# Kernel optimization log

Measured on AMD Instinct MI355X. Metric: run time of the kernel, lower is better.

Reference implementation:

```python
import jax, jax.numpy as jnp
import numpy as np

H = 32        # num query heads
KVH = 8       # num kv heads
D = 128       # head_dim
ROPE_BASE = 10000.0
NEG_INF = jnp.finfo(jnp.float32).min


def rope_interleaved(x):
    """Interleaved (GPT-NeoX-style pairs (x0,x1),(x2,x3),...) RoPE. x: [b,s,h,d]."""
    d = x.shape[-1]
    inv_freq = 1.0 / (ROPE_BASE ** (jnp.arange(0, d, 2, dtype=jnp.float32) / d))  # [d/2]
    pos = jnp.arange(x.shape[1], dtype=jnp.float32)
    ang = pos[:, None] * inv_freq[None, :]                    # [s, d/2]
    cos = jnp.cos(ang)[None, :, None, :]
    sin = jnp.sin(ang)[None, :, None, :]
    xp = x.reshape(*x.shape[:-1], d // 2, 2)
    x1, x2 = xp[..., 0], xp[..., 1]
    r1 = x1 * cos - x2 * sin
    r2 = x1 * sin + x2 * cos
    return jnp.stack([r1, r2], axis=-1).reshape(x.shape)


def setup_inputs() -> dict:
    key = jax.random.key(0)
    k1, k2, k3 = jax.random.split(key, 3)
    B, S, E = 2, 2048, 4096
    x = jax.random.normal(k1, (B, S, E), dtype=jnp.float32)
    wqkv = jax.random.normal(k2, (E + 2 * KVH * D, E), dtype=jnp.float32) * 0.02
    wo = jax.random.normal(k3, (E, E), dtype=jnp.float32) * 0.02
    return {"x": x, "wqkv": wqkv, "wo": wo}


def reference(x, wqkv, wo):
    b, s, e = x.shape
    q_per_kv = H // KVH
    # fused QKV projection (torch Linear layout: y = x @ W.T)
    qkv = jnp.einsum('bse,fe->bsf', x, wqkv)
    # rearrange 'b s (h gs d) -> b s h gs d', gs = q_per_kv + 2
    qkv = qkv.reshape(b, s, KVH, q_per_kv + 2, D)
    q = qkv[..., :q_per_kv, :].reshape(b, s, H, D)   # (h gs) -> H query heads
    k = qkv[..., -2, :]                              # [b,s,KVH,D]
    v = qkv[..., -1, :]
    # RoPE (rotary_emb_dim == head_dim, interleaved)
    q = rope_interleaved(q)
    k = rope_interleaved(k)
    # GQA: expand kv heads to match query heads
    k = jnp.repeat(k, q_per_kv, axis=2)              # [b,s,H,D]
    v = jnp.repeat(v, q_per_kv, axis=2)
    scale = D ** -0.5
    scores = jnp.einsum('bqhd,bkhd->bhqk', q, k) * scale
    causal = jnp.tril(jnp.ones((s, s), dtype=bool))
    scores = jnp.where(causal[None, None], scores, NEG_INF)
    attn = jax.nn.softmax(scores, axis=-1)
    ctx = jnp.einsum('bhqk,bkhd->bqhd', attn, v).reshape(b, s, H * D)
    return jnp.einsum('bsf,ef->bse', ctx, wo)
```

## Files before the change

kernel.cpp:

```cpp
#include <hip/hip_runtime.h>
#include <cstdint>

typedef __bf16 bf16;
typedef __bf16 bf16x8 __attribute__((ext_vector_type(8)));
typedef float  f32x4  __attribute__((ext_vector_type(4)));

#define AS1(p) ((__attribute__((address_space(1))) void*)(p))
#define AS3(p) ((__attribute__((address_space(3))) void*)(p))

__device__ __forceinline__ void gload16(const void* g, void* l) {
  __builtin_amdgcn_global_load_lds(AS1(g), AS3(l), 16, 0, 0);
}

constexpr int B_ = 2, S_ = 2048, E_ = 4096, H_ = 32, KVH_ = 8, D_ = 128;
constexpr int QPK_ = H_ / KVH_;
constexpr int F_ = E_ + 2 * KVH_ * D_;
constexpr int M_ = B_ * S_;

__global__ void f2bf_k(const float* __restrict__ in, bf16* __restrict__ out, int n8) {
  int i = blockIdx.x * 256 + threadIdx.x;
  if (i >= n8) return;
  const float4* p = (const float4*)(in + (size_t)i * 8);
  float4 a = p[0], b = p[1];
  bf16x8 o;
  o[0] = (bf16)a.x; o[1] = (bf16)a.y; o[2] = (bf16)a.z; o[3] = (bf16)a.w;
  o[4] = (bf16)b.x; o[5] = (bf16)b.y; o[6] = (bf16)b.z; o[7] = (bf16)b.w;
  *(bf16x8*)(out + (size_t)i * 8) = o;
}

__global__ void rope_table_k(float2* __restrict__ tab) {
  int i = blockIdx.x * 256 + threadIdx.x;
  int s = i >> 6, f = i & 63;
  float inv = powf(10000.0f, -2.0f * (float)f / 128.0f);
  float ang = (float)s * inv;
  tab[i] = make_float2(cosf(ang), sinf(ang));
}

template <typename OutT>
__global__ __launch_bounds__(512, 2)
void gemm128(const bf16* __restrict__ A, const bf16* __restrict__ B,
             OutT* __restrict__ C, int M, int N, int K) {
  __shared__ bf16 As[3][128 * 64];
  __shared__ bf16 Bs[3][256 * 64];
  const int tid = threadIdx.x;
  const int wid = tid >> 6, lane = tid & 63;
  const int l15 = lane & 15, g = lane >> 4;
  const int wr = wid >> 2, wc = wid & 3;
  const int bm = blockIdx.x, bn = blockIdx.y;
  const bf16* Ab = A + (size_t)bm * 128 * K;
  const bf16* Bb = B + (size_t)bn * 256 * K;
  const int nT = K >> 6;
  const int swzr = (l15 & 7) << 4;

  f32x4 acc[4][4];
#pragma unroll
  for (int m = 0; m < 4; ++m)
#pragma unroll
    for (int n = 0; n < 4; ++n) acc[m][n] = (f32x4){0.f, 0.f, 0.f, 0.f};

  auto stgA = [&](int t) {
    bf16* dst = &As[t % 3][0];
#pragma unroll
    for (int i = 0; i < 2; ++i) {
      int lb = i * 8192 + tid * 16;
      int row = lb >> 7;
      int colb = (lb & 127) ^ ((row & 7) << 4);
      gload16(Ab + (size_t)row * K + t * 64 + (colb >> 1),
              dst + ((i * 8192 + wid * 1024) >> 1));
    }
  };
  auto stgB = [&](int t) {
    bf16* dst = &Bs[t % 3][0];
#pragma unroll
    for (int i = 0; i < 4; ++i) {
      int lb = i * 8192 + tid * 16;
      int row = lb >> 7;
      int colb = (lb & 127) ^ ((row & 7) << 4);
      gload16(Bb + (size_t)row * K + t * 64 + (colb >> 1),
              dst + ((i * 8192 + wid * 1024) >> 1));
    }
  };

  stgA(0); stgB(0);
  if (nT > 1) { stgA(1); stgB(1); asm volatile("s_waitcnt vmcnt(6)"); }
  else        { asm volatile("s_waitcnt vmcnt(0)"); }
  __builtin_amdgcn_sched_barrier(0);
  __builtin_amdgcn_s_barrier();

  bf16x8 af[4][2], blo[2][2], bhi[2][2];
  for (int t = 0; t < nT; ++t) {
    const int cur = t % 3;
#pragma unroll
    for (int m = 0; m < 4; ++m) {
      int arow = wr * 64 + m * 16 + l15;
#pragma unroll
      for (int ks = 0; ks < 2; ++ks)
        af[m][ks] = *(const bf16x8*)&As[cur][(arow << 6) + (((ks * 64 + g * 16) ^ swzr) >> 1)];
    }
#pragma unroll
    for (int n = 0; n < 2; ++n) {
      int brow = wc * 64 + n * 16 + l15;
#pragma unroll
      for (int ks = 0; ks < 2; ++ks)
        blo[n][ks] = *(const bf16x8*)&Bs[cur][(brow << 6) + (((ks * 64 + g * 16) ^ swzr) >> 1)];
    }
    if (t + 2 < nT) stgA(t + 2);
    __builtin_amdgcn_s_barrier();
    asm volatile("s_waitcnt lgkmcnt(0)");
    __builtin_amdgcn_sched_barrier(0);
    __builtin_amdgcn_s_setprio(1);
#pragma unroll
    for (int ks = 0; ks < 2; ++ks)
#pragma unroll
      for (int m = 0; m < 4; ++m)
#pragma unroll
        for (int n = 0; n < 2; ++n)
          acc[m][n] = __builtin_amdgcn_mfma_f32_16x16x32_bf16(af[m][ks], blo[n][ks], acc[m][n], 0, 0, 0);
    __builtin_amdgcn_s_setprio(0);
    __builtin_amdgcn_s_barrier();
#pragma unroll
    for (int n = 0; n < 2; ++n) {
      int brow = wc * 64 + 32 + n * 16 + l15;
#pragma unroll
      for (int ks = 0; ks < 2; ++ks)
        bhi[n][ks] = *(const bf16x8*)&Bs[cur][(brow << 6) + (((ks * 64 + g * 16) ^ swzr) >> 1)];
    }
    if (t + 2 < nT) stgB(t + 2);
    __builtin_amdgcn_s_barrier();
    asm volatile("s_waitcnt lgkmcnt(0)");
    __builtin_amdgcn_sched_barrier(0);
    __builtin_amdgcn_s_setprio(1);
#pragma unroll
    for (int ks = 0; ks < 2; ++ks)
#pragma unroll
      for (int m = 0; m < 4; ++m)
#pragma unroll
        for (int n = 0; n < 2; ++n)
          acc[m][2 + n] = __builtin_amdgcn_mfma_f32_16x16x32_bf16(af[m][ks], bhi[n][ks], acc[m][2 + n], 0, 0, 0);
    __builtin_amdgcn_s_setprio(0);
    if (t + 2 < nT)      { asm volatile("s_waitcnt vmcnt(6)"); }
    else if (t + 1 < nT) { asm volatile("s_waitcnt vmcnt(0)"); }
    __builtin_amdgcn_sched_barrier(0);
    __builtin_amdgcn_s_barrier();
  }

#pragma unroll
  for (int m = 0; m < 4; ++m) {
    int row0 = bm * 128 + wr * 64 + m * 16 + g * 4;
#pragma unroll
    for (int n = 0; n < 4; ++n) {
      int col = bn * 256 + wc * 64 + n * 16 + l15;
      f32x4 v = acc[m][n];
#pragma unroll
      for (int r = 0; r < 4; ++r)
        C[(size_t)(row0 + r) * N + col] = (OutT)v[r];
    }
  }
}

template <typename OutT>
__global__ __launch_bounds__(512, 2)
void gemm256(const bf16* __restrict__ A, const bf16* __restrict__ B,
             OutT* __restrict__ C, int M, int N, int K) {
  __shared__ bf16 As[2][16384];
  __shared__ bf16 Bs[2][16384];
  const int tid = threadIdx.x;
  const int wid = tid >> 6, lane = tid & 63;
  const int l15 = lane & 15, g = lane >> 4;
  const int wr = wid >> 2, wc = wid & 3;
  const int bm = blockIdx.x, bn = blockIdx.y;
  const bf16* Ab = A + (size_t)bm * 256 * K;
  const bf16* Bb = B + (size_t)bn * 256 * K;
  const int nT = K >> 6;
  const int swzr = (l15 & 7) << 4;

  f32x4 acc[8][4];
#pragma unroll
  for (int m = 0; m < 8; ++m)
#pragma unroll
    for (int n = 0; n < 4; ++n) acc[m][n] = (f32x4){0.f, 0.f, 0.f, 0.f};

  auto stg = [&](const bf16* src, bf16* dst, int t, int h) {
#pragma unroll
    for (int i = 0; i < 2; ++i) {
      int lb = h * 16384 + i * 8192 + wid * 1024 + lane * 16;
      int row = lb >> 7;
      int colb = (lb & 127) ^ ((row & 7) << 4);
      gload16(src + (size_t)row * K + t * 64 + (colb >> 1),
              dst + ((h * 16384 + i * 8192 + wid * 1024) >> 1));
    }
  };

  bf16x8 af[4][2];
  bf16x8 bfr[2][2][2];

  stg(Bb, Bs[0], 0, 0); stg(Bb, Bs[0], 0, 1);
  stg(Ab, As[0], 0, 0); stg(Ab, As[0], 0, 1);
  if (nT > 1) {
    stg(Bb, Bs[1], 1, 0); stg(Bb, Bs[1], 1, 1);
    asm volatile("s_waitcnt vmcnt(4)");
  } else {
    asm volatile("s_waitcnt vmcnt(0)");
  }
  __builtin_amdgcn_sched_barrier(0);
  __builtin_amdgcn_s_barrier();

  for (int t = 0; t < nT; ++t) {
    const int cur = t & 1;
#pragma unroll
    for (int m = 0; m < 4; ++m) {
      int arow = wr * 128 + m * 16 + l15;
#pragma unroll
      for (int ks = 0; ks < 2; ++ks)
        af[m][ks] = *(const bf16x8*)&As[cur][(arow << 6) + (((ks * 64 + g * 16) ^ swzr) >> 1)];
    }
#pragma unroll
    for (int n = 0; n < 2; ++n) {
      int brow = wc * 64 + n * 16 + l15;
#pragma unroll
      for (int ks = 0; ks < 2; ++ks)
        bfr[0][n][ks] = *(const bf16x8*)&Bs[cur][(brow << 6) + (((ks * 64 + g * 16) ^ swzr) >> 1)];
    }
    if (t + 1 < nT) stg(Ab, As[cur ^ 1], t + 1, 0);
    __builtin_amdgcn_s_barrier();
    asm volatile("s_waitcnt lgkmcnt(0)");
    __builtin_amdgcn_s_setprio(1);
#pragma unroll
    for (int ks = 0; ks < 2; ++ks)
#pragma unroll
      for (int m = 0; m < 4; ++m)
#pragma unroll
        for (int n = 0; n < 2; ++n)
          acc[m][n] = __builtin_amdgcn_mfma_f32_16x16x32_bf16(af[m][ks], bfr[0][n][ks], acc[m][n], 0, 0, 0);
    __builtin_amdgcn_s_setprio(0);
    __builtin_amdgcn_s_barrier();
#pragma unroll
    for (int n = 0; n < 2; ++n) {
      int brow = wc * 64 + 32 + n * 16 + l15;
#pragma unroll
      for (int ks = 0; ks < 2; ++ks)
        bfr[1][n][ks] = *(const bf16x8*)&Bs[cur][(brow << 6) + (((ks * 64 + g * 16) ^ swzr) >> 1)];
    }
    if (t + 1 < nT) stg(Ab, As[cur ^ 1], t + 1, 1);
    __builtin_amdgcn_s_barrier();
    asm volatile("s_waitcnt lgkmcnt(0)");
    __builtin_amdgcn_s_setprio(1);
#pragma unroll
    for (int ks = 0; ks < 2; ++ks)
#pragma unroll
      for (int m = 0; m < 4; ++m)
#pragma unroll
        for (int n = 0; n < 2; ++n)
          acc[m][2 + n] = __builtin_amdgcn_mfma_f32_16x16x32_bf16(af[m][ks], bfr[1][n][ks], acc[m][2 + n], 0, 0, 0);
    __builtin_amdgcn_s_setprio(0);
    __builtin_amdgcn_s_barrier();
#pragma unroll
    for (int m = 0; m < 4; ++m) {
      int arow = wr * 128 + 64 + m * 16 + l15;
#pragma unroll
      for (int ks = 0; ks < 2; ++ks)
        af[m][ks] = *(const bf16x8*)&As[cur][(arow << 6) + (((ks * 64 + g * 16) ^ swzr) >> 1)];
    }
    if (t + 2 < nT) stg(Bb, Bs[cur], t + 2, 0);
    __builtin_amdgcn_s_barrier();
    asm volatile("s_waitcnt lgkmcnt(0)");
    __builtin_amdgcn_s_setprio(1);
#pragma unroll
    for (int ks = 0; ks < 2; ++ks)
#pragma unroll
      for (int m = 0; m < 4; ++m)
#pragma unroll
        for (int n = 0; n < 2; ++n)
          acc[4 + m][n] = __builtin_amdgcn_mfma_f32_16x16x32_bf16(af[m][ks], bfr[0][n][ks], acc[4 + m][n], 0, 0, 0);
    __builtin_amdgcn_s_setprio(0);
    __builtin_amdgcn_s_barrier();
    if (t + 2 < nT) stg(Bb, Bs[cur], t + 2, 1);
    __builtin_amdgcn_s_setprio(1);
#pragma unroll
    for (int ks = 0; ks < 2; ++ks)
#pragma unroll
      for (int m = 0; m < 4; ++m)
#pragma unroll
        for (int n = 0; n < 2; ++n)
          acc[4 + m][2 + n] = __builtin_amdgcn_mfma_f32_16x16x32_bf16(af[m][ks], bfr[1][n][ks], acc[4 + m][2 + n], 0, 0, 0);
    __builtin_amdgcn_s_setprio(0);
    if (t + 2 < nT)      { asm volatile("s_waitcnt vmcnt(4)"); }
    else if (t + 1 < nT) { asm volatile("s_waitcnt vmcnt(0)"); }
    __builtin_amdgcn_sched_barrier(0);
    __builtin_amdgcn_s_barrier();
  }

#pragma unroll
  for (int mh = 0; mh < 2; ++mh)
#pragma unroll
    for (int m = 0; m < 4; ++m) {
      int row0 = bm * 256 + wr * 128 + mh * 64 + m * 16 + g * 4;
#pragma unroll
      for (int nh = 0; nh < 2; ++nh)
#pragma unroll
        for (int n = 0; n < 2; ++n) {
          int col = bn * 256 + wc * 64 + nh * 32 + n * 16 + l15;
          f32x4 v = acc[mh * 4 + m][nh * 2 + n];
#pragma unroll
          for (int r = 0; r < 4; ++r)
            C[(size_t)(row0 + r) * N + col] = (OutT)v[r];
        }
    }
}

__global__ void rope_q_k(const bf16* __restrict__ qkv, const float2* __restrict__ tab,
                         bf16* __restrict__ qout) {
  int idx = blockIdx.x * 256 + threadIdx.x;
  int c = idx & 15;
  int h = (idx >> 4) & 31;
  int s = (idx >> 9) & 2047;
  int b = idx >> 20;
  int d0 = c * 8;
  int kvh = h >> 2, j = h & 3;
  const bf16* src = qkv + (size_t)(b * 2048 + s) * F_ + kvh * (QPK_ + 2) * D_ + j * D_ + d0;
  bf16x8 v = *(const bf16x8*)src;
  const float2* tb = tab + s * 64 + (d0 >> 1);
  bf16x8 o;
#pragma unroll
  for (int p = 0; p < 4; ++p) {
    float x0 = (float)v[2 * p], x1 = (float)v[2 * p + 1];
    float2 cs = tb[p];
    o[2 * p]     = (bf16)(x0 * cs.x - x1 * cs.y);
    o[2 * p + 1] = (bf16)(x0 * cs.y + x1 * cs.x);
  }
  *(bf16x8*)(qout + (((size_t)b * 2048 + s) * 32 + h) * 128 + d0) = o;
}

__global__ void rope_k_k(const bf16* __restrict__ qkv, const float2* __restrict__ tab,
                         bf16* __restrict__ kout) {
  int idx = blockIdx.x * 256 + threadIdx.x;
  int c = idx & 15;
  int kvh = (idx >> 4) & 7;
  int s = (idx >> 7) & 2047;
  int b = idx >> 18;
  int d0 = c * 8;
  const bf16* src = qkv + (size_t)(b * 2048 + s) * F_ + kvh * (QPK_ + 2) * D_ + QPK_ * D_ + d0;
  bf16x8 v = *(const bf16x8*)src;
  const float2* tb = tab + s * 64 + (d0 >> 1);
  bf16x8 o;
#pragma unroll
  for (int p = 0; p < 4; ++p) {
    float x0 = (float)v[2 * p], x1 = (float)v[2 * p + 1];
    float2 cs = tb[p];
    o[2 * p]     = (bf16)(x0 * cs.x - x1 * cs.y);
    o[2 * p + 1] = (bf16)(x0 * cs.y + x1 * cs.x);
  }
  *(bf16x8*)(kout + ((size_t)(b * 8 + kvh) * 2048 + s) * 128 + d0) = o;
}

__global__ void vtrans_k(const bf16* __restrict__ qkv, bf16* __restrict__ vt) {
  int bidx = blockIdx.x;
  int st = bidx & 31;
  int dt = (bidx >> 5) & 3;
  int kvh = (bidx >> 7) & 7;
  int b = bidx >> 10;
  __shared__ bf16 tile[64][40];
  int t = threadIdx.x;
  {
    int sl = t >> 2, d0 = (t & 3) * 8;
    bf16x8 v = *(const bf16x8*)(qkv + (size_t)(b * 2048 + st * 64 + sl) * F_ +
                                kvh * (QPK_ + 2) * D_ + (QPK_ + 1) * D_ + dt * 32 + d0);
#pragma unroll
    for (int i = 0; i < 8; ++i) tile[sl][d0 + i] = v[i];
  }
  __syncthreads();
  {
    int dl = t >> 3, s0 = (t & 7) * 8;
    bf16x8 o;
#pragma unroll
    for (int i = 0; i < 8; ++i) o[i] = tile[s0 + i][dl];
    *(bf16x8*)(vt + ((size_t)(b * 8 + kvh) * 128 + dt * 32 + dl) * 2048 + st * 64 + s0) = o;
  }
}

__global__ __launch_bounds__(512, 2)
void attn_k(const bf16* __restrict__ q, const bf16* __restrict__ k,
            const bf16* __restrict__ vt, bf16* __restrict__ ctx) {
  int bid = blockIdx.x;
  bid = (bid & 7) * 64 + (bid >> 3);
  int qp = bid & 7;
  int h = (bid >> 3) & 31;
  int b = bid >> 8;
  int kvh = h >> 2;
  int tid = threadIdx.x, w = tid >> 6, lane = tid & 63;
  int l15 = lane & 15, g = lane >> 4;

  __shared__ bf16 Ks[3][64 * 128];
  __shared__ bf16 Vs[3][128 * 64];
  __shared__ bf16 Plds[8][16 * 80];

  bf16* Pw = &Plds[w][0];
  const float C2 = 0.08838834764831845f * 1.4426950408889634f;
  const float NEG = -3.0e38f;

  const bf16* kb_base = k + (size_t)(b * 8 + kvh) * 2048 * 128;
  const bf16* vt_base = vt + (size_t)(b * 8 + kvh) * 128 * 2048;

  auto stage = [&](int kv0, int buf) {
#pragma unroll
    for (int i = 0; i < 2; ++i) {
      int lt = i * 8192 + tid * 16;
      int row = lt >> 8;
      int ch = (lt >> 4) & 15;
      int srcel = (ch ^ (row & 7)) << 3;
      gload16(kb_base + (size_t)(kv0 + row) * 128 + srcel,
              &Ks[buf][(i * 8192 + w * 1024) >> 1]);
    }
#pragma unroll
    for (int i = 0; i < 2; ++i) {
      int lt = i * 8192 + tid * 16;
      int row = lt >> 7;
      int ch = (lt >> 4) & 7;
      int srcel = (ch ^ (row & 7)) << 3;
      gload16(vt_base + (size_t)row * 2048 + kv0 + srcel,
              &Vs[buf][(i * 8192 + w * 1024) >> 1]);
    }
  };

  const int kxor = (l15 & 7) << 4;

  for (int pass = 0; pass < 2; ++pass) {
    int qt = pass ? (15 - qp) : qp;
    int qrow0 = qt * 128 + w * 16;

    bf16x8 aq[4];
#pragma unroll
    for (int ks = 0; ks < 4; ++ks)
      aq[ks] = *(const bf16x8*)(q + (((size_t)b * 2048 + qrow0 + l15) * 32 + h) * 128 + ks * 32 + g * 8);

    f32x4 acco[8];
#pragma unroll
    for (int n = 0; n < 8; ++n) acco[n] = (f32x4){0.f, 0.f, 0.f, 0.f};
    float m_r[4] = {NEG, NEG, NEG, NEG};
    float l_r[4] = {0.f, 0.f, 0.f, 0.f};

    const int nk = 2 * qt + 2;
    stage(0, 0);
    stage(64, 1);
    asm volatile("s_waitcnt vmcnt(4)");
    __builtin_amdgcn_sched_barrier(0);
    __builtin_amdgcn_s_barrier();

    for (int kt = 0; kt < nk; ++kt) {
      int kv0 = kt * 64;
      int cur = kt % 3;
      if (kt + 2 < nk) stage(kv0 + 128, (kt + 2) % 3);

      if (kv0 <= qrow0 + 15) {
        f32x4 s[4];
#pragma unroll
        for (int n = 0; n < 4; ++n) s[n] = (f32x4){0.f, 0.f, 0.f, 0.f};
#pragma unroll
        for (int ks = 0; ks < 4; ++ks) {
          int off = ((ks * 64 + g * 16) ^ kxor) >> 1;
#pragma unroll
          for (int n = 0; n < 4; ++n) {
            bf16x8 kb = *(const bf16x8*)&Ks[cur][(n * 16 + l15) * 128 + off];
            s[n] = __builtin_amdgcn_mfma_f32_16x16x32_bf16(aq[ks], kb, s[n], 0, 0, 0);
          }
        }
        if (kv0 + 63 > qrow0) {
#pragma unroll
          for (int n = 0; n < 4; ++n)
#pragma unroll
            for (int r = 0; r < 4; ++r) {
              int qg = qrow0 + g * 4 + r;
              int kg = kv0 + n * 16 + l15;
              if (kg > qg) s[n][r] = NEG;
            }
        }
        float fac[4];
#pragma unroll
        for (int r = 0; r < 4; ++r) {
          float mx = fmaxf(fmaxf(s[0][r], s[1][r]), fmaxf(s[2][r], s[3][r]));
#pragma unroll
          for (int off = 1; off < 16; off <<= 1) mx = fmaxf(mx, __shfl_xor(mx, off));
          float mn = fmaxf(m_r[r], mx);
          fac[r] = exp2f((m_r[r] - mn) * C2);
          m_r[r] = mn;
        }
        float psum[4] = {0.f, 0.f, 0.f, 0.f};
#pragma unroll
        for (int n = 0; n < 4; ++n)
#pragma unroll
          for (int r = 0; r < 4; ++r) {
            float p = exp2f((s[n][r] - m_r[r]) * C2);
            psum[r] += p;
            Pw[(g * 4 + r) * 80 + n * 16 + l15] = (bf16)p;
          }
#pragma unroll
        for (int r = 0; r < 4; ++r) {
          float ps = psum[r];
#pragma unroll
          for (int off = 1; off < 16; off <<= 1) ps += __shfl_xor(ps, off);
          l_r[r] = l_r[r] * fac[r] + ps;
        }
#pragma unroll
        for (int n = 0; n < 8; ++n)
#pragma unroll
          for (int r = 0; r < 4; ++r) acco[n][r] *= fac[r];
        __builtin_amdgcn_sched_barrier(0);
        asm volatile("s_waitcnt lgkmcnt(0)");
        __builtin_amdgcn_sched_barrier(0);
#pragma unroll
        for (int ks = 0; ks < 2; ++ks) {
          bf16x8 pa = *(const bf16x8*)&Pw[l15 * 80 + ks * 32 + g * 8];
          int off = ((ks * 64 + g * 16) ^ kxor) >> 1;
#pragma unroll
          for (int n = 0; n < 8; ++n) {
            bf16x8 vb = *(const bf16x8*)&Vs[cur][(n * 16 + l15) * 64 + off];
            acco[n] = __builtin_amdgcn_mfma_f32_16x16x32_bf16(pa, vb, acco[n], 0, 0, 0);
          }
        }
      }

      if (kt + 1 < nk) {
        if (kt + 2 < nk) { asm volatile("s_waitcnt vmcnt(4)"); }
        else             { asm volatile("s_waitcnt vmcnt(0)"); }
        __builtin_amdgcn_sched_barrier(0);
      }
      __builtin_amdgcn_s_barrier();
    }

#pragma unroll
    for (int r = 0; r < 4; ++r) {
      float inv = 1.0f / l_r[r];
      int qg = qrow0 + g * 4 + r;
#pragma unroll
      for (int n = 0; n < 8; ++n)
        ctx[(((size_t)b * 2048 + qg) * 32 + h) * 128 + n * 16 + l15] = (bf16)(acco[n][r] * inv);
    }
  }
}

extern "C" void kernel_launch(void* const* d_in, const int* in_sizes, int n_in,
                              void* d_out, int out_size, void* d_ws, size_t ws_size,
                              hipStream_t stream) {
  const float* x = (const float*)d_in[0];
  const float* wqkv = (const float*)d_in[1];
  const float* wo = (const float*)d_in[2];
  float* out = (float*)d_out;
  char* ws = (char*)d_ws;

  bf16* xbf    = (bf16*)(ws + 0);
  bf16* wqkvbf = (bf16*)(ws + 33554432);
  bf16* qkvbf  = (bf16*)(ws + 83886080);
  bf16* qbuf   = (bf16*)(ws + 134217728);
  bf16* kbuf   = (bf16*)(ws + 167772160);
  bf16* vtbuf  = (bf16*)(ws + 176160768);
  float2* tab  = (float2*)(ws + 184549376);

  f2bf_k<<<8192, 256, 0, stream>>>(x, xbf, M_ * E_ / 8);
  f2bf_k<<<12288, 256, 0, stream>>>(wqkv, wqkvbf, F_ * E_ / 8);
  rope_table_k<<<512, 256, 0, stream>>>(tab);

  gemm128<bf16><<<dim3(M_ / 128, F_ / 256), 512, 0, stream>>>(xbf, wqkvbf, qkvbf, M_, F_, E_);

  rope_q_k<<<8192, 256, 0, stream>>>(qkvbf, tab, qbuf);
  rope_k_k<<<2048, 256, 0, stream>>>(qkvbf, tab, kbuf);
  vtrans_k<<<2048, 256, 0, stream>>>(qkvbf, vtbuf);

  bf16* wobf = qkvbf;
  f2bf_k<<<8192, 256, 0, stream>>>(wo, wobf, E_ * E_ / 8);

  bf16* ctx = xbf;
  attn_k<<<512, 512, 0, stream>>>(qbuf, kbuf, vtbuf, ctx);

  gemm256<float><<<dim3(M_ / 256, E_ / 256), 512, 0, stream>>>(ctx, wobf, out, M_, E_, E_);
}
```

Measured before the change: 595.8 us.

## Retile QKV GEMM to 256x192, fuse prologue kernels, pad P LDS stride

Replaces the 128x256 QKV projection GEMM with a 256x192 tile that double-buffers A and triple-buffers B, raising arithmetic intensity per block. It merges the x and wqkv bf16 conversions and the RoPE table build into one launch to cut launch overhead. It also unrolls the output-projection K loop by two and changes the attention P scratch stride to reduce LDS bank conflicts. The larger tiles increase LDS and register use, which may lower occupancy. The new stride also misaligns 16-byte LDS reads.

```diff
diff --git a/kernel.cpp b/kernel.cpp
--- a/kernel.cpp
+++ b/kernel.cpp
@@ -17,9 +17,9 @@
 constexpr int F_ = E_ + 2 * KVH_ * D_;
 constexpr int M_ = B_ * S_;
 
-__global__ void f2bf_k(const float* __restrict__ in, bf16* __restrict__ out, int n8) {
-  int i = blockIdx.x * 256 + threadIdx.x;
-  if (i >= n8) return;
+constexpr int PST = 84;
+
+__device__ __forceinline__ void conv8(const float* in, bf16* out, int i) {
   const float4* p = (const float4*)(in + (size_t)i * 8);
   float4 a = p[0], b = p[1];
   bf16x8 o;
@@ -28,41 +28,58 @@
   *(bf16x8*)(out + (size_t)i * 8) = o;
 }
 
-__global__ void rope_table_k(float2* __restrict__ tab) {
+__global__ void init_k(const float* __restrict__ x, bf16* __restrict__ xbf,
+                       const float* __restrict__ wqkv, bf16* __restrict__ wqkvbf,
+                       float2* __restrict__ tab) {
   int i = blockIdx.x * 256 + threadIdx.x;
-  int s = i >> 6, f = i & 63;
-  float inv = powf(10000.0f, -2.0f * (float)f / 128.0f);
-  float ang = (float)s * inv;
-  tab[i] = make_float2(cosf(ang), sinf(ang));
+  if (i < 2097152) {
+    conv8(x, xbf, i);
+  } else if (i < 2097152 + 3145728) {
+    conv8(wqkv, wqkvbf, i - 2097152);
+  } else {
+    int j = i - 5242880;
+    if (j < 131072) {
+      int s = j >> 6, f = j & 63;
+      float inv = powf(10000.0f, -2.0f * (float)f / 128.0f);
+      float ang = (float)s * inv;
+      tab[j] = make_float2(cosf(ang), sinf(ang));
+    }
+  }
+}
+
+__global__ void f2bf_k(const float* __restrict__ in, bf16* __restrict__ out, int n8) {
+  int i = blockIdx.x * 256 + threadIdx.x;
+  if (i >= n8) return;
+  conv8(in, out, i);
 }
 
 template <typename OutT>
 __global__ __launch_bounds__(512, 2)
-void gemm128(const bf16* __restrict__ A, const bf16* __restrict__ B,
+void gemm192(const bf16* __restrict__ A, const bf16* __restrict__ B,
              OutT* __restrict__ C, int M, int N, int K) {
-  __shared__ bf16 As[3][128 * 64];
-  __shared__ bf16 Bs[3][256 * 64];
+  __shared__ bf16 As[2][256 * 64];
+  __shared__ bf16 Bs[3][192 * 64];
   const int tid = threadIdx.x;
   const int wid = tid >> 6, lane = tid & 63;
   const int l15 = lane & 15, g = lane >> 4;
   const int wr = wid >> 2, wc = wid & 3;
   const int bm = blockIdx.x, bn = blockIdx.y;
-  const bf16* Ab = A + (size_t)bm * 128 * K;
-  const bf16* Bb = B + (size_t)bn * 256 * K;
+  const bf16* Ab = A + (size_t)bm * 256 * K;
+  const bf16* Bb = B + (size_t)bn * 192 * K;
   const int nT = K >> 6;
   const int swzr = (l15 & 7) << 4;
 
-  f32x4 acc[4][4];
-#pragma unroll
-  for (int m = 0; m < 4; ++m)
-#pragma unroll
-    for (int n = 0; n < 4; ++n) acc[m][n] = (f32x4){0.f, 0.f, 0.f, 0.f};
+  f32x4 acc[8][3];
+#pragma unroll
+  for (int m = 0; m < 8; ++m)
+#pragma unroll
+    for (int n = 0; n < 3; ++n) acc[m][n] = (f32x4){0.f, 0.f, 0.f, 0.f};
 
   auto stgA = [&](int t) {
-    bf16* dst = &As[t % 3][0];
-#pragma unroll
-    for (int i = 0; i < 2; ++i) {
-      int lb = i * 8192 + tid * 16;
+    bf16* dst = &As[t & 1][0];
+#pragma unroll
+    for (int i = 0; i < 4; ++i) {
+      int lb = i * 8192 + wid * 1024 + lane * 16;
       int row = lb >> 7;
       int colb = (lb & 127) ^ ((row & 7) << 4);
       gload16(Ab + (size_t)row * K + t * 64 + (colb >> 1),
@@ -72,8 +89,8 @@
   auto stgB = [&](int t) {
     bf16* dst = &Bs[t % 3][0];
 #pragma unroll
-    for (int i = 0; i < 4; ++i) {
-      int lb = i * 8192 + tid * 16;
+    for (int i = 0; i < 3; ++i) {
+      int lb = i * 8192 + wid * 1024 + lane * 16;
       int row = lb >> 7;
       int colb = (lb & 127) ^ ((row & 7) << 4);
       gload16(Bb + (size_t)row * K + t * 64 + (colb >> 1),
@@ -82,29 +99,30 @@
   };
 
   stgA(0); stgB(0);
-  if (nT > 1) { stgA(1); stgB(1); asm volatile("s_waitcnt vmcnt(6)"); }
+  if (nT > 1) { stgB(1); asm volatile("s_waitcnt vmcnt(3)"); }
   else        { asm volatile("s_waitcnt vmcnt(0)"); }
   __builtin_amdgcn_sched_barrier(0);
   __builtin_amdgcn_s_barrier();
 
-  bf16x8 af[4][2], blo[2][2], bhi[2][2];
+  bf16x8 af[4][2], bfr[3][2];
   for (int t = 0; t < nT; ++t) {
-    const int cur = t % 3;
+    const bf16* Asc = &As[t & 1][0];
+    const bf16* Bsc = &Bs[t % 3][0];
 #pragma unroll
     for (int m = 0; m < 4; ++m) {
-      int arow = wr * 64 + m * 16 + l15;
-#pragma unroll
-      for (int ks = 0; ks < 2; ++ks)
-        af[m][ks] = *(const bf16x8*)&As[cur][(arow << 6) + (((ks * 64 + g * 16) ^ swzr) >> 1)];
-    }
-#pragma unroll
-    for (int n = 0; n < 2; ++n) {
-      int brow = wc * 64 + n * 16 + l15;
-#pragma unroll
-      for (int ks = 0; ks < 2; ++ks)
-        blo[n][ks] = *(const bf16x8*)&Bs[cur][(brow << 6) + (((ks * 64 + g * 16) ^ swzr) >> 1)];
-    }
-    if (t + 2 < nT) stgA(t + 2);
+      int arow = wr * 128 + m * 16 + l15;
+#pragma unroll
+      for (int ks = 0; ks < 2; ++ks)
+        af[m][ks] = *(const bf16x8*)&Asc[(arow << 6) + (((ks * 64 + g * 16) ^ swzr) >> 1)];
+    }
+#pragma unroll
+    for (int n = 0; n < 3; ++n) {
+      int brow = wc * 48 + n * 16 + l15;
+#pragma unroll
+      for (int ks = 0; ks < 2; ++ks)
+        bfr[n][ks] = *(const bf16x8*)&Bsc[(brow << 6) + (((ks * 64 + g * 16) ^ swzr) >> 1)];
+    }
+    if (t + 1 < nT) stgA(t + 1);
     __builtin_amdgcn_s_barrier();
     asm volatile("s_waitcnt lgkmcnt(0)");
     __builtin_amdgcn_sched_barrier(0);
@@ -114,16 +132,16 @@
 #pragma unroll
       for (int m = 0; m < 4; ++m)
 #pragma unroll
-        for (int n = 0; n < 2; ++n)
-          acc[m][n] = __builtin_amdgcn_mfma_f32_16x16x32_bf16(af[m][ks], blo[n][ks], acc[m][n], 0, 0, 0);
+        for (int n = 0; n < 3; ++n)
+          acc[m][n] = __builtin_amdgcn_mfma_f32_16x16x32_bf16(af[m][ks], bfr[n][ks], acc[m][n], 0, 0, 0);
     __builtin_amdgcn_s_setprio(0);
     __builtin_amdgcn_s_barrier();
 #pragma unroll
-    for (int n = 0; n < 2; ++n) {
-      int brow = wc * 64 + 32 + n * 16 + l15;
-#pragma unroll
-      for (int ks = 0; ks < 2; ++ks)
-        bhi[n][ks] = *(const bf16x8*)&Bs[cur][(brow << 6) + (((ks * 64 + g * 16) ^ swzr) >> 1)];
+    for (int m = 0; m < 4; ++m) {
+      int arow = wr * 128 + 64 + m * 16 + l15;
+#pragma unroll
+      for (int ks = 0; ks < 2; ++ks)
+        af[m][ks] = *(const bf16x8*)&Asc[(arow << 6) + (((ks * 64 + g * 16) ^ swzr) >> 1)];
     }
     if (t + 2 < nT) stgB(t + 2);
     __builtin_amdgcn_s_barrier();
@@ -135,21 +153,21 @@
 #pragma unroll
       for (int m = 0; m < 4; ++m)
 #pragma unroll
-        for (int n = 0; n < 2; ++n)
-          acc[m][2 + n] = __builtin_amdgcn_mfma_f32_16x16x32_bf16(af[m][ks], bhi[n][ks], acc[m][2 + n], 0, 0, 0);
+        for (int n = 0; n < 3; ++n)
+          acc[4 + m][n] = __builtin_amdgcn_mfma_f32_16x16x32_bf16(af[m][ks], bfr[n][ks], acc[4 + m][n], 0, 0, 0);
     __builtin_amdgcn_s_setprio(0);
-    if (t + 2 < nT)      { asm volatile("s_waitcnt vmcnt(6)"); }
+    if (t + 2 < nT)      { asm volatile("s_waitcnt vmcnt(3)"); }
     else if (t + 1 < nT) { asm volatile("s_waitcnt vmcnt(0)"); }
     __builtin_amdgcn_sched_barrier(0);
     __builtin_amdgcn_s_barrier();
   }
 
 #pragma unroll
-  for (int m = 0; m < 4; ++m) {
-    int row0 = bm * 128 + wr * 64 + m * 16 + g * 4;
-#pragma unroll
-    for (int n = 0; n < 4; ++n) {
-      int col = bn * 256 + wc * 64 + n * 16 + l15;
+  for (int m = 0; m < 8; ++m) {
+    int row0 = bm * 256 + wr * 128 + m * 16 + g * 4;
+#pragma unroll
+    for (int n = 0; n < 3; ++n) {
+      int col = bn * 192 + wc * 48 + n * 16 + l15;
       f32x4 v = acc[m][n];
 #pragma unroll
       for (int r = 0; r < 4; ++r)
@@ -205,8 +223,7 @@
   __builtin_amdgcn_sched_barrier(0);
   __builtin_amdgcn_s_barrier();
 
-  for (int t = 0; t < nT; ++t) {
-    const int cur = t & 1;
+  auto tileK = [&](int t, const int cur) {
 #pragma unroll
     for (int m = 0; m < 4; ++m) {
       int arow = wr * 128 + m * 16 + l15;
@@ -288,6 +305,11 @@
     else if (t + 1 < nT) { asm volatile("s_waitcnt vmcnt(0)"); }
     __builtin_amdgcn_sched_barrier(0);
     __builtin_amdgcn_s_barrier();
+  };
+
+  for (int tt = 0; tt < nT; tt += 2) {
+    tileK(tt, 0);
+    tileK(tt + 1, 1);
   }
 
 #pragma unroll
@@ -392,7 +414,7 @@
 
   __shared__ bf16 Ks[3][64 * 128];
   __shared__ bf16 Vs[3][128 * 64];
-  __shared__ bf16 Plds[8][16 * 80];
+  __shared__ bf16 Plds[8][16 * PST];
 
   bf16* Pw = &Plds[w][0];
   const float C2 = 0.08838834764831845f * 1.4426950408889634f;
@@ -491,7 +513,7 @@
           for (int r = 0; r < 4; ++r) {
             float p = exp2f((s[n][r] - m_r[r]) * C2);
             psum[r] += p;
-            Pw[(g * 4 + r) * 80 + n * 16 + l15] = (bf16)p;
+            Pw[(g * 4 + r) * PST + n * 16 + l15] = (bf16)p;
           }
 #pragma unroll
         for (int r = 0; r < 4; ++r) {
@@ -509,7 +531,7 @@
         __builtin_amdgcn_sched_barrier(0);
 #pragma unroll
         for (int ks = 0; ks < 2; ++ks) {
-          bf16x8 pa = *(const bf16x8*)&Pw[l15 * 80 + ks * 32 + g * 8];
+          bf16x8 pa = *(const bf16x8*)&Pw[l15 * PST + ks * 32 + g * 8];
           int off = ((ks * 64 + g * 16) ^ kxor) >> 1;
 #pragma unroll
           for (int n = 0; n < 8; ++n) {
@@ -555,11 +577,9 @@
   bf16* vtbuf  = (bf16*)(ws + 176160768);
   float2* tab  = (float2*)(ws + 184549376);
 
-  f2bf_k<<<8192, 256, 0, stream>>>(x, xbf, M_ * E_ / 8);
-  f2bf_k<<<12288, 256, 0, stream>>>(wqkv, wqkvbf, F_ * E_ / 8);
-  rope_table_k<<<512, 256, 0, stream>>>(tab);
-
-  gemm128<bf16><<<dim3(M_ / 128, F_ / 256), 512, 0, stream>>>(xbf, wqkvbf, qkvbf, M_, F_, E_);
+  init_k<<<20992, 256, 0, stream>>>(x, xbf, wqkv, wqkvbf, tab);
+
+  gemm192<bf16><<<dim3(M_ / 256, F_ / 192), 512, 0, stream>>>(xbf, wqkvbf, qkvbf, M_, F_, E_);
 
   rope_q_k<<<8192, 256, 0, stream>>>(qkvbf, tab, qbuf);
   rope_k_k<<<2048, 256, 0, stream>>>(qkvbf, tab, kbuf);
```

Measured after the change: 572.7 us. -3.9%, faster.
